# Optimization experiments

Measured on AMD Instinct MI355X. Metric: run time of the kernel, lower is better.

The kernel has to match this reference:

```python
import jax, jax.numpy as jnp
import numpy as np

D_MODEL = 2048
D_INNER = 2048
D_XB = 512
N_HEADS = 32
HEADDIM = 64   # P
DSTATE = 64    # N
N_KV = D_XB // DSTATE          # 8 kv heads
REP = N_HEADS // N_KV
D_FF = 8192
DCONV = 4
EPS = 1e-5
B, L = 1, 2048


def _rmsnorm(x, w, eps=EPS):
    return x * jax.lax.rsqrt(jnp.mean(x * x, axis=-1, keepdims=True) + eps) * w


def _silu(x):
    return x * jax.nn.sigmoid(x)


def _causal_dwconv(x, w, b):
    # x: (B,L,C), depthwise causal conv, kernel DCONV
    xp = jnp.pad(x, ((0, 0), (DCONV - 1, 0), (0, 0)))
    y = b
    for k in range(DCONV):  # small fixed kernel loop
        y = y + xp[:, k:k + x.shape[1], :] * w[:, k]
    return y


def setup_inputs() -> dict:
    key = jax.random.key(0)
    ks = jax.random.split(key, 10)
    s = 0.02
    d_proj = 2 * D_INNER + 2 * D_XB + N_HEADS  # z, x, B, C, dt
    conv_ch = 2 * D_XB + D_INNER               # conv over concat(x, B, C)
    return {
        "hidden_states": jax.random.normal(ks[0], (B, L, D_MODEL), jnp.float32),
        "in_proj_w": jax.random.normal(ks[1], (d_proj, D_MODEL), jnp.float32) * s,
        "conv_w": jax.random.normal(ks[2], (conv_ch, DCONV), jnp.float32) * s,
        "conv_b": jnp.zeros((conv_ch,), jnp.float32),
        "dt_bias": jax.random.normal(ks[3], (N_HEADS,), jnp.float32) * s,
        "A_log": jnp.log(jnp.arange(1, N_HEADS + 1, dtype=jnp.float32)),
        "D": jnp.ones((N_HEADS,), jnp.float32),
        "ssm_norm_w": jnp.ones((D_INNER,), jnp.float32),
        "out_proj_w": jax.random.normal(ks[4], (D_MODEL, D_INNER), jnp.float32) * s,
        "input_ln_w": jnp.ones((D_MODEL,), jnp.float32),
        "post_ln_w": jnp.ones((D_MODEL,), jnp.float32),
        "gate_w": jax.random.normal(ks[5], (D_FF, D_MODEL), jnp.float32) * s,
        "up_w": jax.random.normal(ks[6], (D_FF, D_MODEL), jnp.float32) * s,
        "down_w": jax.random.normal(ks[7], (D_MODEL, D_FF), jnp.float32) * s,
    }


def _mamba2(hs, in_proj_w, conv_w, conv_b, dt_bias, A_log, D, ssm_norm_w, out_proj_w):
    b, l, _ = hs.shape
    zxbcdt = hs @ in_proj_w.T
    z, x, Bm, Cm, dt = jnp.split(
        zxbcdt, [D_INNER, D_INNER + D_XB, D_INNER + 2 * D_XB, 2 * D_INNER + 2 * D_XB], axis=-1)
    # causal depthwise conv + silu over concat(x, B, C)
    xBC = _silu(_causal_dwconv(jnp.concatenate([x, Bm, Cm], axis=-1), conv_w, conv_b))
    x, Bm, Cm = jnp.split(xBC, [D_XB, 2 * D_XB], axis=-1)
    # heads (GQA: repeat x and B from N_KV to N_HEADS)
    x = jnp.repeat(x.reshape(b, l, N_KV, HEADDIM), REP, axis=2)      # (b,l,H,P)
    Bm = jnp.repeat(Bm.reshape(b, l, N_KV, DSTATE), REP, axis=2)     # (b,l,H,N)
    Cm = Cm.reshape(b, l, N_HEADS, DSTATE)                            # (b,l,H,N)
    dt = jax.nn.softplus(dt + dt_bias)                                # (b,l,H)
    dA = jnp.exp(dt * (-jnp.exp(A_log)))                              # (b,l,H)
    # selective scan over time
    xs = (jnp.moveaxis(dA, 1, 0), jnp.moveaxis(dt, 1, 0),
          jnp.moveaxis(x, 1, 0), jnp.moveaxis(Bm, 1, 0), jnp.moveaxis(Cm, 1, 0))
    h0 = jnp.zeros((b, N_HEADS, HEADDIM, DSTATE), hs.dtype)

    def step(h, t):
        dA_t, dt_t, x_t, B_t, C_t = t
        h = h * dA_t[:, :, None, None] + jnp.einsum('bh,bhp,bhn->bhpn', dt_t, x_t, B_t)
        y = jnp.einsum('bhpn,bhn->bhp', h, C_t)
        return h, y

    _, ys = jax.lax.scan(step, h0, xs)            # (l,b,H,P)
    y = jnp.moveaxis(ys, 0, 1) + D[None, None, :, None] * x
    y = y.reshape(b, l, D_INNER)
    y = _rmsnorm(y * _silu(z), ssm_norm_w)        # gated RMSNorm
    return y @ out_proj_w.T


def reference(hidden_states, in_proj_w, conv_w, conv_b, dt_bias, A_log, D,
              ssm_norm_w, out_proj_w, input_ln_w, post_ln_w, gate_w, up_w, down_w):
    residual = hidden_states
    h = _rmsnorm(hidden_states, input_ln_w)
    h = residual + _mamba2(h, in_proj_w, conv_w, conv_b, dt_bias, A_log, D,
                           ssm_norm_w, out_proj_w)
    residual = h
    h = _rmsnorm(h, post_ln_w)
    h = (_silu(h @ gate_w.T) * (h @ up_w.T)) @ down_w.T
    return residual + h
```

## Files before the change

### kernel.cpp

```cpp
#include <hip/hip_runtime.h>

typedef unsigned short u16;
typedef unsigned int u32;
typedef float f32x4 __attribute__((ext_vector_type(4)));
typedef __bf16 bf16x8 __attribute__((ext_vector_type(8)));
typedef unsigned short u16x8 __attribute__((ext_vector_type(8)));

#define L_SEQ 2048
#define DMODEL 2048
#define DINNER 2048
#define DXB 512
#define NHEADS 32
#define DPROJ 5152
#define DPROJ_PAD 5376
#define CONVCH 3072
#define DFF 8192
#define NCHUNK 32
#define CHUNK 64

__device__ __forceinline__ float bf2f(u16 u) {
  union { unsigned int i; float f; } v; v.i = ((unsigned int)u) << 16; return v.f;
}
__device__ __forceinline__ u16 f2bf(float f) {
  union { float f; unsigned int i; } v; v.f = f;
  unsigned int u = v.i;
  u += 0x7FFFu + ((u >> 16) & 1u);
  return (u16)(u >> 16);
}
__device__ __forceinline__ float siluf(float x) { return x / (1.f + __expf(-x)); }

#define GL16(gsrc, ldst) \
  __builtin_amdgcn_global_load_lds((const __attribute__((address_space(1))) u32*)(gsrc), \
                                   (__attribute__((address_space(3))) u32*)(ldst), 16, 0, 0)
#define SBAR() __builtin_amdgcn_s_barrier()
#define WAIT_VM4() asm volatile("s_waitcnt vmcnt(4)" ::: "memory")
#define WAIT_VM0() asm volatile("s_waitcnt vmcnt(0)" ::: "memory")

__global__ __launch_bounds__(256) void cvt_k(
    const float* __restrict__ s, u16* __restrict__ d, int n8)
{
  const int i = blockIdx.x * 256 + threadIdx.x;
  if (i >= n8) return;
  f32x4 a = *(const f32x4*)(s + (size_t)i * 8);
  f32x4 b = *(const f32x4*)(s + (size_t)i * 8 + 4);
  u16x8 o;
#pragma unroll
  for (int j = 0; j < 4; ++j) { o[j] = f2bf(a[j]); o[j + 4] = f2bf(b[j]); }
  *(u16x8*)(d + (size_t)i * 8) = o;
}

__global__ __launch_bounds__(256) void cvt_pad_k(
    const float* __restrict__ s, u16* __restrict__ d)
{
  const int i = blockIdx.x * 256 + threadIdx.x;
  const int row = (i * 8) >> 11;
  u16x8 o;
  if (row < DPROJ) {
    f32x4 a = *(const f32x4*)(s + (size_t)i * 8);
    f32x4 b = *(const f32x4*)(s + (size_t)i * 8 + 4);
#pragma unroll
    for (int j = 0; j < 4; ++j) { o[j] = f2bf(a[j]); o[j + 4] = f2bf(b[j]); }
  } else {
#pragma unroll
    for (int j = 0; j < 8; ++j) o[j] = 0;
  }
  *(u16x8*)(d + (size_t)i * 8) = o;
}

template<int MH, int NH>
__device__ __forceinline__ void mfma16(f32x4 (&acc)[8][4], const bf16x8 (&af)[4][2],
                                       const bf16x8 (&bfq)[2][2][2]) {
#pragma unroll
  for (int s = 0; s < 2; ++s)
#pragma unroll
    for (int m = 0; m < 4; ++m)
#pragma unroll
      for (int n = 0; n < 2; ++n)
        acc[MH * 4 + m][NH * 2 + n] = __builtin_amdgcn_mfma_f32_16x16x32_bf16(
            af[m][s], bfq[NH][n][s], acc[MH * 4 + m][NH * 2 + n], 0, 0, 0);
}

template<int EPI, int SPLIT>
__global__ __launch_bounds__(512, 2) void gemm8(
    const u16* __restrict__ A, const u16* __restrict__ W,
    void* __restrict__ Cptr, const u16* __restrict__ gateB,
    const int N, const int K, const int gx)
{
  __shared__ u16 sm[65536];
  const int tid = threadIdx.x;
  const int wid = tid >> 6, ln = tid & 63;
  const int wm = wid >> 2, wn = wid & 3;

  const int nwg = gridDim.x;
  int wg = (int)blockIdx.x;
  wg = (wg & 7) * (nwg >> 3) + (wg >> 3);
  const int tilesPerZ = gx << 3;
  const int bz = wg / tilesPerZ;
  const int rem = wg - bz * tilesPerZ;
  const int bx = rem >> 3;
  const int by = rem & 7;
  const int m0 = by << 8, n0 = bx << 8;
  const int NT = (K >> 6) / SPLIT;
  const int ktB = bz * NT;

  f32x4 acc[8][4];
#pragma unroll
  for (int i = 0; i < 8; ++i)
#pragma unroll
    for (int j = 0; j < 4; ++j) acc[i][j] = f32x4{0.f, 0.f, 0.f, 0.f};

  const int l8r = ln >> 3;
  const int schunk = (ln & 7) ^ l8r;
  const int lr16 = ln & 15;
  const int q4 = ln >> 4;
  const int swz = ln & 7;
  const int c0 = ((q4 ^ swz) << 3);

  auto stageA = [&](int buf, int kt, int h) {
#pragma unroll
    for (int g = 0; g < 2; ++g) {
      const int rr = (wid << 3) + l8r;
      const size_t grow = (size_t)(m0 + (g << 7) + (h << 6) + rr);
      const u16* src = A + grow * K + (size_t)((ktB + kt) << 6) + (schunk << 3);
      u16* dst = &sm[(buf << 15) + (((h << 7) + (g << 6) + (wid << 3)) << 6)];
      GL16(src, dst);
    }
  };
  auto stageB = [&](int buf, int kt, int h) {
#pragma unroll
    for (int g = 0; g < 2; ++g) {
      const int v = (g << 6) + (wid << 3) + l8r;
      const int grow = n0 + ((v >> 5) << 6) + (h << 5) + (v & 31);
      const u16* src = W + (size_t)grow * K + (size_t)((ktB + kt) << 6) + (schunk << 3);
      u16* dst = &sm[(buf << 15) + 16384 + (((h << 7) + (g << 6) + (wid << 3)) << 6)];
      GL16(src, dst);
    }
  };

  bf16x8 af[4][2], bfq[2][2][2];
  auto loadA = [&](int buf, int mh) {
#pragma unroll
    for (int m = 0; m < 4; ++m) {
      const int lrA = (mh << 7) + (wm << 6) + (m << 4) + lr16;
      const u16* p = &sm[(buf << 15) + (lrA << 6)];
      af[m][0] = *(const bf16x8*)(p + c0);
      af[m][1] = *(const bf16x8*)(p + (c0 ^ 32));
    }
  };
  auto loadB = [&](int buf, int nh) {
#pragma unroll
    for (int n = 0; n < 2; ++n) {
      const int lrB = (nh << 7) + (wn << 5) + (n << 4) + lr16;
      const u16* p = &sm[(buf << 15) + 16384 + (lrB << 6)];
      bfq[nh][n][0] = *(const bf16x8*)(p + c0);
      bfq[nh][n][1] = *(const bf16x8*)(p + (c0 ^ 32));
    }
  };

  stageA(0, 0, 0); stageA(0, 0, 1); stageB(0, 0, 0); stageB(0, 0, 1);
  stageA(1, 1, 0); stageB(1, 1, 1);
  WAIT_VM4();
  SBAR();

  for (int kt = 0; kt < NT; kt += 2) {
    const bool s2 = (kt + 2) < NT, s3 = (kt + 3) < NT;
    loadA(0, 0); loadB(0, 0);
    stageA(1, kt + 1, 1);
    __builtin_amdgcn_s_setprio(1); mfma16<0, 0>(acc, af, bfq); __builtin_amdgcn_s_setprio(0);
    SBAR();
    loadB(0, 1);
    stageB(1, kt + 1, 0);
    __builtin_amdgcn_s_setprio(1); mfma16<0, 1>(acc, af, bfq); __builtin_amdgcn_s_setprio(0);
    SBAR();
    loadA(0, 1);
    if (s2) stageA(0, kt + 2, 0);
    __builtin_amdgcn_s_setprio(1); mfma16<1, 1>(acc, af, bfq); __builtin_amdgcn_s_setprio(0);
    SBAR();
    if (s2) stageB(0, kt + 2, 1);
    __builtin_amdgcn_s_setprio(1); mfma16<1, 0>(acc, af, bfq); __builtin_amdgcn_s_setprio(0);
    if (s2) { WAIT_VM4(); } else { WAIT_VM0(); }
    SBAR();
    loadA(1, 0); loadB(1, 0);
    if (s2) stageA(0, kt + 2, 1);
    __builtin_amdgcn_s_setprio(1); mfma16<0, 0>(acc, af, bfq); __builtin_amdgcn_s_setprio(0);
    SBAR();
    loadB(1, 1);
    if (s2) stageB(0, kt + 2, 0);
    __builtin_amdgcn_s_setprio(1); mfma16<0, 1>(acc, af, bfq); __builtin_amdgcn_s_setprio(0);
    SBAR();
    loadA(1, 1);
    if (s3) stageA(1, kt + 3, 0);
    __builtin_amdgcn_s_setprio(1); mfma16<1, 1>(acc, af, bfq); __builtin_amdgcn_s_setprio(0);
    SBAR();
    if (s3) stageB(1, kt + 3, 1);
    __builtin_amdgcn_s_setprio(1); mfma16<1, 0>(acc, af, bfq); __builtin_amdgcn_s_setprio(0);
    if (s2) { if (s3) { WAIT_VM4(); } else { WAIT_VM0(); } }
    SBAR();
  }

  const int crow0 = m0 + (wm << 7) + (q4 << 2);
  const int ccol0 = n0 + (wn << 6) + lr16;
#pragma unroll
  for (int M = 0; M < 8; ++M) {
#pragma unroll
    for (int n = 0; n < 4; ++n) {
      const int col = ccol0 + (n << 4);
      if (col < N) {
#pragma unroll
        for (int j = 0; j < 4; ++j) {
          const size_t idx = (size_t)(crow0 + (M << 4) + j) * N + col;
          if (EPI == 0) {
            ((u16*)Cptr)[idx] = f2bf(acc[M][n][j]);
          } else if (EPI == 2) {
            float* P = (float*)Cptr + (size_t)bz * ((size_t)L_SEQ * N);
            P[idx] = acc[M][n][j];
          } else {
            ((u16*)Cptr)[idx] = f2bf(siluf(bf2f(gateB[idx])) * acc[M][n][j]);
          }
        }
      }
    }
  }
}

__global__ __launch_bounds__(256) void rmsnorm_k(
    const float* __restrict__ in, const float* __restrict__ w, u16* __restrict__ out)
{
  const int row = blockIdx.x, tid = threadIdx.x;
  const float* r = in + (size_t)row * DMODEL + tid * 8;
  f32x4 v0 = *(const f32x4*)r;
  f32x4 v1 = *(const f32x4*)(r + 4);
  float ss = v0[0]*v0[0] + v0[1]*v0[1] + v0[2]*v0[2] + v0[3]*v0[3]
           + v1[0]*v1[0] + v1[1]*v1[1] + v1[2]*v1[2] + v1[3]*v1[3];
#pragma unroll
  for (int off = 1; off < 64; off <<= 1) ss += __shfl_xor(ss, off);
  __shared__ float part[4];
  if ((tid & 63) == 0) part[tid >> 6] = ss;
  __syncthreads();
  const float tot = part[0] + part[1] + part[2] + part[3];
  const float scale = rsqrtf(tot * (1.f / DMODEL) + 1e-5f);
  f32x4 w0 = *(const f32x4*)(w + tid * 8);
  f32x4 w1 = *(const f32x4*)(w + tid * 8 + 4);
  u16x8 o;
#pragma unroll
  for (int j = 0; j < 4; ++j) {
    o[j]     = f2bf(v0[j] * scale * w0[j]);
    o[j + 4] = f2bf(v1[j] * scale * w1[j]);
  }
  *(u16x8*)(out + (size_t)row * DMODEL + tid * 8) = o;
}

__global__ __launch_bounds__(256) void red4_rms_k(
    const float* __restrict__ P, const float* __restrict__ resid,
    float* __restrict__ hres, const float* __restrict__ w, u16* __restrict__ h2)
{
  const int row = blockIdx.x, tid = threadIdx.x;
  const size_t base = (size_t)row * DMODEL + tid * 8;
  const size_t stride = (size_t)L_SEQ * DMODEL;
  f32x4 v0 = *(const f32x4*)(resid + base);
  f32x4 v1 = *(const f32x4*)(resid + base + 4);
#pragma unroll
  for (int p = 0; p < 4; ++p) {
    v0 += *(const f32x4*)(P + p * stride + base);
    v1 += *(const f32x4*)(P + p * stride + base + 4);
  }
  *(f32x4*)(hres + base) = v0;
  *(f32x4*)(hres + base + 4) = v1;
  float ss = v0[0]*v0[0] + v0[1]*v0[1] + v0[2]*v0[2] + v0[3]*v0[3]
           + v1[0]*v1[0] + v1[1]*v1[1] + v1[2]*v1[2] + v1[3]*v1[3];
#pragma unroll
  for (int off = 1; off < 64; off <<= 1) ss += __shfl_xor(ss, off);
  __shared__ float part[4];
  if ((tid & 63) == 0) part[tid >> 6] = ss;
  __syncthreads();
  const float tot = part[0] + part[1] + part[2] + part[3];
  const float scale = rsqrtf(tot * (1.f / DMODEL) + 1e-5f);
  f32x4 w0 = *(const f32x4*)(w + tid * 8);
  f32x4 w1 = *(const f32x4*)(w + tid * 8 + 4);
  u16x8 o;
#pragma unroll
  for (int j = 0; j < 4; ++j) {
    o[j]     = f2bf(v0[j] * scale * w0[j]);
    o[j + 4] = f2bf(v1[j] * scale * w1[j]);
  }
  *(u16x8*)(h2 + base) = o;
}

__global__ __launch_bounds__(256) void red4_add_k(
    const float* __restrict__ P, const float* __restrict__ resid, float* __restrict__ out)
{
  const size_t base = ((size_t)blockIdx.x * 256 + threadIdx.x) * 8;
  const size_t stride = (size_t)L_SEQ * DMODEL;
  f32x4 v0 = *(const f32x4*)(resid + base);
  f32x4 v1 = *(const f32x4*)(resid + base + 4);
#pragma unroll
  for (int p = 0; p < 4; ++p) {
    v0 += *(const f32x4*)(P + p * stride + base);
    v1 += *(const f32x4*)(P + p * stride + base + 4);
  }
  *(f32x4*)(out + base) = v0;
  *(f32x4*)(out + base + 4) = v1;
}

__global__ __launch_bounds__(256) void gated_rms_k(
    const float* __restrict__ y, const u16* __restrict__ zx,
    const float* __restrict__ w, u16* __restrict__ out)
{
  const int row = blockIdx.x, tid = threadIdx.x;
  const float* yr = y + (size_t)row * DINNER + tid * 8;
  f32x4 y0 = *(const f32x4*)yr;
  f32x4 y1 = *(const f32x4*)(yr + 4);
  u16x8 zv = *(const u16x8*)(zx + (size_t)row * DPROJ + tid * 8);
  float val[8];
#pragma unroll
  for (int j = 0; j < 4; ++j) {
    val[j]     = y0[j] * siluf(bf2f(zv[j]));
    val[j + 4] = y1[j] * siluf(bf2f(zv[j + 4]));
  }
  float ss = 0.f;
#pragma unroll
  for (int j = 0; j < 8; ++j) ss += val[j] * val[j];
#pragma unroll
  for (int off = 1; off < 64; off <<= 1) ss += __shfl_xor(ss, off);
  __shared__ float part[4];
  if ((tid & 63) == 0) part[tid >> 6] = ss;
  __syncthreads();
  const float tot = part[0] + part[1] + part[2] + part[3];
  const float scale = rsqrtf(tot * (1.f / DINNER) + 1e-5f);
  u16x8 o;
#pragma unroll
  for (int j = 0; j < 8; ++j) o[j] = f2bf(val[j] * scale * w[tid * 8 + j]);
  *(u16x8*)(out + (size_t)row * DINNER + tid * 8) = o;
}

__global__ __launch_bounds__(256) void conv_k(
    const u16* __restrict__ zx, const float* __restrict__ w,
    const float* __restrict__ b, u16* __restrict__ xbc)
{
  const int flat = blockIdx.x * 256 + threadIdx.x;
  const int t = flat / 384;
  const int c8 = (flat % 384) * 8;
  float acc[8];
  f32x4 b0 = *(const f32x4*)(b + c8);
  f32x4 b1 = *(const f32x4*)(b + c8 + 4);
#pragma unroll
  for (int j = 0; j < 4; ++j) { acc[j] = b0[j]; acc[j + 4] = b1[j]; }
  f32x4 wr[8];
#pragma unroll
  for (int j = 0; j < 8; ++j) wr[j] = *(const f32x4*)(w + (size_t)(c8 + j) * 4);
#pragma unroll
  for (int k = 0; k < 4; ++k) {
    const int tt = t - 3 + k;
    if (tt >= 0) {
      u16x8 xv = *(const u16x8*)(zx + (size_t)tt * DPROJ + DINNER + c8);
#pragma unroll
      for (int j = 0; j < 8; ++j) acc[j] += bf2f(xv[j]) * wr[j][k];
    }
  }
  u16x8 o;
#pragma unroll
  for (int j = 0; j < 8; ++j) o[j] = f2bf(siluf(acc[j]));
  *(u16x8*)(xbc + (size_t)t * CONVCH + c8) = o;
}

__global__ __launch_bounds__(256) void dt_k(
    const u16* __restrict__ zx, const float* __restrict__ dt_bias,
    const float* __restrict__ A_log, float* __restrict__ dtv, float* __restrict__ dAv)
{
  const int flat = blockIdx.x * 256 + threadIdx.x;
  const int t = flat >> 5, h = flat & 31;
  const float x = bf2f(zx[(size_t)t * DPROJ + (DPROJ - NHEADS) + h]) + dt_bias[h];
  const float sp = (x > 20.f) ? x : log1pf(expf(x));
  const float a = expf(A_log[h]);
  dtv[flat] = sp;
  dAv[flat] = expf(-a * sp);
}

__device__ __forceinline__ void stage16(float* dst, const u16* src) {
  u16x8 a = *(const u16x8*)src;
  u16x8 b = *(const u16x8*)(src + 8);
#pragma unroll
  for (int j = 0; j < 8; ++j) { dst[j] = bf2f(a[j]); dst[8 + j] = bf2f(b[j]); }
}

__global__ __launch_bounds__(256) void scan_a(
    const u16* __restrict__ xbc, const float* __restrict__ dtv,
    const float* __restrict__ dAv, const float* __restrict__ Dvec,
    float* __restrict__ y, float* __restrict__ S,
    float* __restrict__ gam, float* __restrict__ cum)
{
  __shared__ float xs[64][64], Bs[64][64], Cs[64][64];
  __shared__ float dts[64], dAs[64];
  const int c = blockIdx.x, h = blockIdx.y, kv = h >> 2;
  const int tid = threadIdx.x;
  const int t0 = c * CHUNK;
  {
    const int r = tid >> 2, cq = (tid & 3) * 16;
    const u16* base = xbc + (size_t)(t0 + r) * CONVCH;
    stage16(&xs[r][cq], base + kv * 64 + cq);
    stage16(&Bs[r][cq], base + DXB + kv * 64 + cq);
    stage16(&Cs[r][cq], base + 2 * DXB + h * 64 + cq);
    if (tid < 64) {
      dts[tid] = dtv[(size_t)(t0 + tid) * NHEADS + h];
      dAs[tid] = dAv[(size_t)(t0 + tid) * NHEADS + h];
    }
  }
  __syncthreads();
  const int p = tid >> 2, q = tid & 3;
  float hreg[16];
#pragma unroll
  for (int i = 0; i < 16; ++i) hreg[i] = 0.f;
  float cumv = 1.f;
  const float Dh = Dvec[h];
  for (int t = 0; t < CHUNK; ++t) {
    const float dtt = dts[t], dat = dAs[t];
    const float xv = xs[t][p];
    const float u = dtt * xv;
    float a0 = 0.f, a1 = 0.f, a2 = 0.f, a3 = 0.f;
#pragma unroll
    for (int i4 = 0; i4 < 4; ++i4) {
      f32x4 b4 = *(const f32x4*)&Bs[t][q * 16 + i4 * 4];
      f32x4 c4 = *(const f32x4*)&Cs[t][q * 16 + i4 * 4];
#pragma unroll
      for (int j = 0; j < 4; ++j) {
        const int i = i4 * 4 + j;
        hreg[i] = hreg[i] * dat + u * b4[j];
        if (i4 == 0) a0 += hreg[i] * c4[j];
        else if (i4 == 1) a1 += hreg[i] * c4[j];
        else if (i4 == 2) a2 += hreg[i] * c4[j];
        else a3 += hreg[i] * c4[j];
      }
    }
    float accv = (a0 + a1) + (a2 + a3);
    accv += __shfl_xor(accv, 1);
    accv += __shfl_xor(accv, 2);
    cumv *= dat;
    if (q == 0) y[(size_t)(t0 + t) * DINNER + h * 64 + p] = accv + Dh * xv;
    if (tid == 0) cum[(size_t)(t0 + t) * NHEADS + h] = cumv;
  }
  float* Sp = S + ((size_t)(c * NHEADS + h) << 12) + tid * 16;
#pragma unroll
  for (int i4 = 0; i4 < 4; ++i4)
    *(f32x4*)(Sp + i4 * 4) = f32x4{hreg[i4*4], hreg[i4*4+1], hreg[i4*4+2], hreg[i4*4+3]};
  if (tid == 0) gam[c * NHEADS + h] = cumv;
}

__global__ __launch_bounds__(256) void scan_b(
    const float* __restrict__ S, const float* __restrict__ gam, float* __restrict__ H)
{
  const int h = blockIdx.x, tid = threadIdx.x;
  float hr[16];
#pragma unroll
  for (int i = 0; i < 16; ++i) hr[i] = 0.f;
  for (int c = 0; c < NCHUNK; ++c) {
    const size_t base = ((size_t)(c * NHEADS + h) << 12) + tid * 16;
#pragma unroll
    for (int i4 = 0; i4 < 4; ++i4)
      *(f32x4*)(H + base + i4 * 4) = f32x4{hr[i4*4], hr[i4*4+1], hr[i4*4+2], hr[i4*4+3]};
    const float g = gam[c * NHEADS + h];
#pragma unroll
    for (int i4 = 0; i4 < 4; ++i4) {
      f32x4 s = *(const f32x4*)(S + base + i4 * 4);
#pragma unroll
      for (int j = 0; j < 4; ++j) hr[i4 * 4 + j] = g * hr[i4 * 4 + j] + s[j];
    }
  }
}

__global__ __launch_bounds__(256) void scan_c(
    const u16* __restrict__ xbc, const float* __restrict__ cum,
    const float* __restrict__ H, float* __restrict__ y)
{
  __shared__ float Cs[64][64];
  __shared__ float cums[64];
  const int c = blockIdx.x, h = blockIdx.y, tid = threadIdx.x;
  const int t0 = c * CHUNK;
  {
    const int r = tid >> 2, cq = (tid & 3) * 16;
    stage16(&Cs[r][cq], xbc + (size_t)(t0 + r) * CONVCH + 2 * DXB + h * 64 + cq);
    if (tid < 64) cums[tid] = cum[(size_t)(t0 + tid) * NHEADS + h];
  }
  const int p = tid >> 2, q = tid & 3;
  float hr[16];
  const size_t base = ((size_t)(c * NHEADS + h) << 12) + tid * 16;
#pragma unroll
  for (int i4 = 0; i4 < 4; ++i4) {
    f32x4 v = *(const f32x4*)(H + base + i4 * 4);
#pragma unroll
    for (int j = 0; j < 4; ++j) hr[i4 * 4 + j] = v[j];
  }
  __syncthreads();
  for (int t = 0; t < CHUNK; ++t) {
    float accv = 0.f;
#pragma unroll
    for (int i4 = 0; i4 < 4; ++i4) {
      f32x4 c4 = *(const f32x4*)&Cs[t][q * 16 + i4 * 4];
#pragma unroll
      for (int j = 0; j < 4; ++j) accv += hr[i4 * 4 + j] * c4[j];
    }
    accv += __shfl_xor(accv, 1);
    accv += __shfl_xor(accv, 2);
    if (q == 0) {
      const size_t idx = (size_t)(t0 + t) * DINNER + h * 64 + p;
      y[idx] += cums[t] * accv;
    }
  }
}

extern "C" void kernel_launch(void* const* d_in, const int* in_sizes, int n_in,
                              void* d_out, int out_size, void* d_ws, size_t ws_size,
                              hipStream_t stream) {
  const float* hs         = (const float*)d_in[0];
  const float* in_proj_w  = (const float*)d_in[1];
  const float* conv_w     = (const float*)d_in[2];
  const float* conv_b     = (const float*)d_in[3];
  const float* dt_bias    = (const float*)d_in[4];
  const float* A_log      = (const float*)d_in[5];
  const float* Dv         = (const float*)d_in[6];
  const float* ssm_w      = (const float*)d_in[7];
  const float* out_proj_w = (const float*)d_in[8];
  const float* in_ln_w    = (const float*)d_in[9];
  const float* post_ln_w  = (const float*)d_in[10];
  const float* gate_w     = (const float*)d_in[11];
  const float* up_w       = (const float*)d_in[12];
  const float* down_w     = (const float*)d_in[13];
  float* out = (float*)d_out;

  char* ws = (char*)d_ws;
  size_t off = 0;
  auto alloc = [&](size_t bytes) -> void* {
    void* p = ws + off;
    off = (off + bytes + 255) & ~(size_t)255;
    return p;
  };
  u16* wip = (u16*)alloc((size_t)DPROJ_PAD * DMODEL * 2);
  u16* wop = (u16*)alloc((size_t)DMODEL * DINNER * 2);
  u16* wg  = (u16*)alloc((size_t)DFF    * DMODEL * 2);
  u16* wu  = (u16*)alloc((size_t)DFF    * DMODEL * 2);
  u16* wd  = (u16*)alloc((size_t)DMODEL * DFF    * 2);
  u16*   zx  = (u16*)  alloc((size_t)L_SEQ * DPROJ * 2);
  u16*   xbc = (u16*)  alloc((size_t)L_SEQ * CONVCH * 2);
  float* Sv  = (float*)alloc((size_t)NCHUNK * NHEADS * 4096 * 4);
  float* Hv  = (float*)alloc((size_t)NCHUNK * NHEADS * 4096 * 4);
  float* pK  = (float*)zx;
  float* dtv = (float*)alloc((size_t)L_SEQ * NHEADS * 4);
  float* dAv = (float*)alloc((size_t)L_SEQ * NHEADS * 4);
  float* cum = (float*)alloc((size_t)L_SEQ * NHEADS * 4);
  float* gam = (float*)alloc((size_t)NCHUNK * NHEADS * 4);
  float* yv  = (float*)alloc((size_t)L_SEQ * DINNER * 4);
  float* hres= (float*)alloc((size_t)L_SEQ * DMODEL * 4);
  u16*  gateb= (u16*)  alloc((size_t)L_SEQ * DFF * 2);
  u16*  hslot= (u16*)  alloc((size_t)L_SEQ * DMODEL * 2);
  (void)ws_size; (void)in_sizes; (void)n_in; (void)out_size;

  cvt_pad_k<<<(DPROJ_PAD * DMODEL / 8) / 256, 256, 0, stream>>>(in_proj_w, wip);
  cvt_k<<<DMODEL * DINNER / 8 / 256, 256, 0, stream>>>(out_proj_w, wop, DMODEL * DINNER / 8);
  cvt_k<<<DFF * DMODEL / 8 / 256, 256, 0, stream>>>(gate_w, wg, DFF * DMODEL / 8);
  cvt_k<<<DFF * DMODEL / 8 / 256, 256, 0, stream>>>(up_w, wu, DFF * DMODEL / 8);
  cvt_k<<<DMODEL * DFF / 8 / 256, 256, 0, stream>>>(down_w, wd, DMODEL * DFF / 8);

  rmsnorm_k<<<L_SEQ, 256, 0, stream>>>(hs, in_ln_w, hslot);
  gemm8<0, 1><<<21 * 8, 512, 0, stream>>>(hslot, wip, zx, nullptr, DPROJ, DMODEL, 21);
  conv_k<<<(L_SEQ * (CONVCH / 8)) / 256, 256, 0, stream>>>(zx, conv_w, conv_b, xbc);
  dt_k<<<(L_SEQ * NHEADS) / 256, 256, 0, stream>>>(zx, dt_bias, A_log, dtv, dAv);
  scan_a<<<dim3(NCHUNK, NHEADS), 256, 0, stream>>>(xbc, dtv, dAv, Dv, yv, Sv, gam, cum);
  scan_b<<<NHEADS, 256, 0, stream>>>(Sv, gam, Hv);
  scan_c<<<dim3(NCHUNK, NHEADS), 256, 0, stream>>>(xbc, cum, Hv, yv);
  gated_rms_k<<<L_SEQ, 256, 0, stream>>>(yv, zx, ssm_w, hslot);
  gemm8<2, 4><<<8 * 8 * 4, 512, 0, stream>>>(hslot, wop, pK, nullptr, DMODEL, DINNER, 8);
  red4_rms_k<<<L_SEQ, 256, 0, stream>>>(pK, hs, hres, post_ln_w, hslot);
  gemm8<0, 1><<<32 * 8, 512, 0, stream>>>(hslot, wg, gateb, nullptr, DFF, DMODEL, 32);
  gemm8<3, 1><<<32 * 8, 512, 0, stream>>>(hslot, wu, gateb, gateb, DFF, DMODEL, 32);
  gemm8<2, 4><<<8 * 8 * 4, 512, 0, stream>>>(gateb, wd, pK, nullptr, DMODEL, DFF, 8);
  red4_add_k<<<(L_SEQ * DMODEL / 8) / 256, 256, 0, stream>>>(pK, hres, out);
}
```

Before: 525.6 us.

## Fuse fp32-to-bf16 weight conversion into GEMM B-tile staging

Drops the five separate weight conversion kernels and their bf16 workspace copies. The GEMM now loads fp32 weight tiles into registers, converts them to bf16, and writes them to LDS itself, replacing the async global-to-LDS DMA for B. The pipeline is reorganised so the loads and LDS writes happen one tile ahead, with full vmcnt/lgkmcnt waits. This removes one write and re-read of about 150 MB of weights in exchange for doubled B-load bytes inside each GEMM, extra VGPR pressure, and less async overlap. Rows past N are clamped instead of zero-padded.

```diff
diff --git a/kernel.cpp b/kernel.cpp
--- a/kernel.cpp
+++ b/kernel.cpp
@@ -12,7 +12,6 @@
 #define DXB 512
 #define NHEADS 32
 #define DPROJ 5152
-#define DPROJ_PAD 5376
 #define CONVCH 3072
 #define DFF 8192
 #define NCHUNK 32
@@ -33,39 +32,8 @@
   __builtin_amdgcn_global_load_lds((const __attribute__((address_space(1))) u32*)(gsrc), \
                                    (__attribute__((address_space(3))) u32*)(ldst), 16, 0, 0)
 #define SBAR() __builtin_amdgcn_s_barrier()
-#define WAIT_VM4() asm volatile("s_waitcnt vmcnt(4)" ::: "memory")
 #define WAIT_VM0() asm volatile("s_waitcnt vmcnt(0)" ::: "memory")
-
-__global__ __launch_bounds__(256) void cvt_k(
-    const float* __restrict__ s, u16* __restrict__ d, int n8)
-{
-  const int i = blockIdx.x * 256 + threadIdx.x;
-  if (i >= n8) return;
-  f32x4 a = *(const f32x4*)(s + (size_t)i * 8);
-  f32x4 b = *(const f32x4*)(s + (size_t)i * 8 + 4);
-  u16x8 o;
-#pragma unroll
-  for (int j = 0; j < 4; ++j) { o[j] = f2bf(a[j]); o[j + 4] = f2bf(b[j]); }
-  *(u16x8*)(d + (size_t)i * 8) = o;
-}
-
-__global__ __launch_bounds__(256) void cvt_pad_k(
-    const float* __restrict__ s, u16* __restrict__ d)
-{
-  const int i = blockIdx.x * 256 + threadIdx.x;
-  const int row = (i * 8) >> 11;
-  u16x8 o;
-  if (row < DPROJ) {
-    f32x4 a = *(const f32x4*)(s + (size_t)i * 8);
-    f32x4 b = *(const f32x4*)(s + (size_t)i * 8 + 4);
-#pragma unroll
-    for (int j = 0; j < 4; ++j) { o[j] = f2bf(a[j]); o[j + 4] = f2bf(b[j]); }
-  } else {
-#pragma unroll
-    for (int j = 0; j < 8; ++j) o[j] = 0;
-  }
-  *(u16x8*)(d + (size_t)i * 8) = o;
-}
+#define WAIT_LGKM0() asm volatile("s_waitcnt lgkmcnt(0)" ::: "memory")
 
 template<int MH, int NH>
 __device__ __forceinline__ void mfma16(f32x4 (&acc)[8][4], const bf16x8 (&af)[4][2],
@@ -82,7 +50,7 @@
 
 template<int EPI, int SPLIT>
 __global__ __launch_bounds__(512, 2) void gemm8(
-    const u16* __restrict__ A, const u16* __restrict__ W,
+    const u16* __restrict__ A, const float* __restrict__ W,
     void* __restrict__ Cptr, const u16* __restrict__ gateB,
     const int N, const int K, const int gx)
 {
@@ -126,14 +94,30 @@
       GL16(src, dst);
     }
   };
-  auto stageB = [&](int buf, int kt, int h) {
-#pragma unroll
-    for (int g = 0; g < 2; ++g) {
-      const int v = (g << 6) + (wid << 3) + l8r;
-      const int grow = n0 + ((v >> 5) << 6) + (h << 5) + (v & 31);
-      const u16* src = W + (size_t)grow * K + (size_t)((ktB + kt) << 6) + (schunk << 3);
-      u16* dst = &sm[(buf << 15) + 16384 + (((h << 7) + (g << 6) + (wid << 3)) << 6)];
-      GL16(src, dst);
+
+  const int brow0 = tid >> 3;
+  const int bcdst = tid & 7;
+  const int bcsrc = bcdst ^ (brow0 & 7);
+  f32x4 breg[4][2];
+  auto bglb = [&](int kt) {
+#pragma unroll
+    for (int t = 0; t < 4; ++t) {
+      int rw = n0 + brow0 + t * 64; rw = rw < N ? rw : N - 1;
+      const float* src = W + (size_t)rw * K + (size_t)((ktB + kt) << 6) + (bcsrc << 3);
+      breg[t][0] = *(const f32x4*)src;
+      breg[t][1] = *(const f32x4*)(src + 4);
+    }
+  };
+  auto bwrite = [&](int buf) {
+#pragma unroll
+    for (int t = 0; t < 4; ++t) {
+      u16x8 bv;
+#pragma unroll
+      for (int j = 0; j < 4; ++j) {
+        bv[j]     = f2bf(breg[t][0][j]);
+        bv[j + 4] = f2bf(breg[t][1][j]);
+      }
+      *(u16x8*)&sm[(buf << 15) + 16384 + ((brow0 + t * 64) << 6) + (bcdst << 3)] = bv;
     }
   };
 
@@ -150,51 +134,54 @@
   auto loadB = [&](int buf, int nh) {
 #pragma unroll
     for (int n = 0; n < 2; ++n) {
-      const int lrB = (nh << 7) + (wn << 5) + (n << 4) + lr16;
+      const int lrB = (wn << 6) + (nh << 5) + (n << 4) + lr16;
       const u16* p = &sm[(buf << 15) + 16384 + (lrB << 6)];
       bfq[nh][n][0] = *(const bf16x8*)(p + c0);
       bfq[nh][n][1] = *(const bf16x8*)(p + (c0 ^ 32));
     }
   };
 
-  stageA(0, 0, 0); stageA(0, 0, 1); stageB(0, 0, 0); stageB(0, 0, 1);
-  stageA(1, 1, 0); stageB(1, 1, 1);
-  WAIT_VM4();
+  bglb(0);
+  stageA(0, 0, 0); stageA(0, 0, 1);
+  bwrite(0);
+  WAIT_VM0();
+  WAIT_LGKM0();
   SBAR();
 
   for (int kt = 0; kt < NT; kt += 2) {
-    const bool s2 = (kt + 2) < NT, s3 = (kt + 3) < NT;
+    const bool s2 = (kt + 2) < NT;
     loadA(0, 0); loadB(0, 0);
+    bglb(kt + 1);
+    stageA(1, kt + 1, 0);
+    __builtin_amdgcn_s_setprio(1); mfma16<0, 0>(acc, af, bfq); __builtin_amdgcn_s_setprio(0);
+    SBAR();
+    loadB(0, 1);
     stageA(1, kt + 1, 1);
+    __builtin_amdgcn_s_setprio(1); mfma16<0, 1>(acc, af, bfq); __builtin_amdgcn_s_setprio(0);
+    SBAR();
+    loadA(0, 1);
+    bwrite(1);
+    __builtin_amdgcn_s_setprio(1); mfma16<1, 1>(acc, af, bfq); __builtin_amdgcn_s_setprio(0);
+    WAIT_LGKM0();
+    SBAR();
+    __builtin_amdgcn_s_setprio(1); mfma16<1, 0>(acc, af, bfq); __builtin_amdgcn_s_setprio(0);
+    WAIT_VM0();
+    SBAR();
+    loadA(1, 0); loadB(1, 0);
+    if (s2) { bglb(kt + 2); stageA(0, kt + 2, 0); }
     __builtin_amdgcn_s_setprio(1); mfma16<0, 0>(acc, af, bfq); __builtin_amdgcn_s_setprio(0);
     SBAR();
-    loadB(0, 1);
-    stageB(1, kt + 1, 0);
+    loadB(1, 1);
+    if (s2) stageA(0, kt + 2, 1);
     __builtin_amdgcn_s_setprio(1); mfma16<0, 1>(acc, af, bfq); __builtin_amdgcn_s_setprio(0);
     SBAR();
-    loadA(0, 1);
-    if (s2) stageA(0, kt + 2, 0);
+    loadA(1, 1);
+    if (s2) bwrite(0);
     __builtin_amdgcn_s_setprio(1); mfma16<1, 1>(acc, af, bfq); __builtin_amdgcn_s_setprio(0);
-    SBAR();
-    if (s2) stageB(0, kt + 2, 1);
+    WAIT_LGKM0();
+    SBAR();
     __builtin_amdgcn_s_setprio(1); mfma16<1, 0>(acc, af, bfq); __builtin_amdgcn_s_setprio(0);
-    if (s2) { WAIT_VM4(); } else { WAIT_VM0(); }
-    SBAR();
-    loadA(1, 0); loadB(1, 0);
-    if (s2) stageA(0, kt + 2, 1);
-    __builtin_amdgcn_s_setprio(1); mfma16<0, 0>(acc, af, bfq); __builtin_amdgcn_s_setprio(0);
-    SBAR();
-    loadB(1, 1);
-    if (s2) stageB(0, kt + 2, 0);
-    __builtin_amdgcn_s_setprio(1); mfma16<0, 1>(acc, af, bfq); __builtin_amdgcn_s_setprio(0);
-    SBAR();
-    loadA(1, 1);
-    if (s3) stageA(1, kt + 3, 0);
-    __builtin_amdgcn_s_setprio(1); mfma16<1, 1>(acc, af, bfq); __builtin_amdgcn_s_setprio(0);
-    SBAR();
-    if (s3) stageB(1, kt + 3, 1);
-    __builtin_amdgcn_s_setprio(1); mfma16<1, 0>(acc, af, bfq); __builtin_amdgcn_s_setprio(0);
-    if (s2) { if (s3) { WAIT_VM4(); } else { WAIT_VM0(); } }
+    WAIT_VM0();
     SBAR();
   }
 
@@ -533,11 +520,6 @@
     off = (off + bytes + 255) & ~(size_t)255;
     return p;
   };
-  u16* wip = (u16*)alloc((size_t)DPROJ_PAD * DMODEL * 2);
-  u16* wop = (u16*)alloc((size_t)DMODEL * DINNER * 2);
-  u16* wg  = (u16*)alloc((size_t)DFF    * DMODEL * 2);
-  u16* wu  = (u16*)alloc((size_t)DFF    * DMODEL * 2);
-  u16* wd  = (u16*)alloc((size_t)DMODEL * DFF    * 2);
   u16*   zx  = (u16*)  alloc((size_t)L_SEQ * DPROJ * 2);
   u16*   xbc = (u16*)  alloc((size_t)L_SEQ * CONVCH * 2);
   float* Sv  = (float*)alloc((size_t)NCHUNK * NHEADS * 4096 * 4);
@@ -553,24 +535,18 @@
   u16*  hslot= (u16*)  alloc((size_t)L_SEQ * DMODEL * 2);
   (void)ws_size; (void)in_sizes; (void)n_in; (void)out_size;
 
-  cvt_pad_k<<<(DPROJ_PAD * DMODEL / 8) / 256, 256, 0, stream>>>(in_proj_w, wip);
-  cvt_k<<<DMODEL * DINNER / 8 / 256, 256, 0, stream>>>(out_proj_w, wop, DMODEL * DINNER / 8);
-  cvt_k<<<DFF * DMODEL / 8 / 256, 256, 0, stream>>>(gate_w, wg, DFF * DMODEL / 8);
-  cvt_k<<<DFF * DMODEL / 8 / 256, 256, 0, stream>>>(up_w, wu, DFF * DMODEL / 8);
-  cvt_k<<<DMODEL * DFF / 8 / 256, 256, 0, stream>>>(down_w, wd, DMODEL * DFF / 8);
-
   rmsnorm_k<<<L_SEQ, 256, 0, stream>>>(hs, in_ln_w, hslot);
-  gemm8<0, 1><<<21 * 8, 512, 0, stream>>>(hslot, wip, zx, nullptr, DPROJ, DMODEL, 21);
+  gemm8<0, 1><<<21 * 8, 512, 0, stream>>>(hslot, in_proj_w, zx, nullptr, DPROJ, DMODEL, 21);
   conv_k<<<(L_SEQ * (CONVCH / 8)) / 256, 256, 0, stream>>>(zx, conv_w, conv_b, xbc);
   dt_k<<<(L_SEQ * NHEADS) / 256, 256, 0, stream>>>(zx, dt_bias, A_log, dtv, dAv);
   scan_a<<<dim3(NCHUNK, NHEADS), 256, 0, stream>>>(xbc, dtv, dAv, Dv, yv, Sv, gam, cum);
   scan_b<<<NHEADS, 256, 0, stream>>>(Sv, gam, Hv);
   scan_c<<<dim3(NCHUNK, NHEADS), 256, 0, stream>>>(xbc, cum, Hv, yv);
   gated_rms_k<<<L_SEQ, 256, 0, stream>>>(yv, zx, ssm_w, hslot);
-  gemm8<2, 4><<<8 * 8 * 4, 512, 0, stream>>>(hslot, wop, pK, nullptr, DMODEL, DINNER, 8);
+  gemm8<2, 4><<<8 * 8 * 4, 512, 0, stream>>>(hslot, out_proj_w, pK, nullptr, DMODEL, DINNER, 8);
   red4_rms_k<<<L_SEQ, 256, 0, stream>>>(pK, hs, hres, post_ln_w, hslot);
-  gemm8<0, 1><<<32 * 8, 512, 0, stream>>>(hslot, wg, gateb, nullptr, DFF, DMODEL, 32);
-  gemm8<3, 1><<<32 * 8, 512, 0, stream>>>(hslot, wu, gateb, gateb, DFF, DMODEL, 32);
-  gemm8<2, 4><<<8 * 8 * 4, 512, 0, stream>>>(gateb, wd, pK, nullptr, DMODEL, DFF, 8);
+  gemm8<0, 1><<<32 * 8, 512, 0, stream>>>(hslot, gate_w, gateb, nullptr, DFF, DMODEL, 32);
+  gemm8<3, 1><<<32 * 8, 512, 0, stream>>>(hslot, up_w, gateb, gateb, DFF, DMODEL, 32);
+  gemm8<2, 4><<<8 * 8 * 4, 512, 0, stream>>>(gateb, down_w, pK, nullptr, DMODEL, DFF, 8);
   red4_add_k<<<(L_SEQ * DMODEL / 8) / 256, 256, 0, stream>>>(pK, hres, out);
 }
```

Measured after the change: 1.078 ms. 2.05x slower.
